# Optimization experiments

Hardware: AMD Instinct MI355X
Metric: run time of the kernel (lower is better)

The kernel has to match this reference:

```python
import math
import jax, jax.numpy as jnp
import numpy as np
from jax import lax

MUL = 16           # multiplicity of 0e and 1o in input and output irreps
NRB = 8            # num_radial_basis
DIAMETER = 3.0
STEPS = (1.0, 1.0, 1.0)
DIM = 4 * MUL      # 16 scalars + 16 vectors * 3 = 64 channels


def _constants():
    # lattice from __init__: arange(-s, s+1) * step per axis, s = floor(r/step)
    r = DIAMETER / 2
    axes = [np.arange(-math.floor(r / st), math.floor(r / st) + 1.0) * st for st in STEPS]
    lattice = np.stack(np.meshgrid(*axes, indexing='ij'), axis=-1)  # [Kx,Ky,Kz,3]
    d = np.linalg.norm(lattice, axis=-1)                            # [Kx,Ky,Kz]
    # soft_one_hot_linspace(basis='smooth_finite', cutoff=True)
    values = np.linspace(0.0, r, NRB + 2)[1:-1]
    step = values[1] - values[0]
    diff = (d[..., None] - values) / step
    inside = diff ** 2 < 1.0
    emb = np.where(inside, 1.14136 * np.exp(2.0) * np.exp(-2.0 / np.where(inside, 1.0 - diff ** 2, 1.0)), 0.0)
    # spherical harmonics, normalize=True, normalization='component'
    n = lattice / np.maximum(d[..., None], 1e-12)  # unit vectors; 0 at the origin voxel
    sh0 = np.ones_like(d)                          # Y_0 (component normalized)
    sh1 = np.sqrt(3.0) * n                         # Y_1 (component normalized)
    return emb.astype(np.float32), sh0.astype(np.float32), sh1.astype(np.float32)

EMB, SH0, SH1 = _constants()
KX, KY, KZ = SH0.shape  # 3,3,3


def setup_inputs() -> dict:
    key = jax.random.key(0)
    ks = jax.random.split(key, 7)
    B, G = 4, 32
    return {
        'x': jax.random.normal(ks[0], (B, G, G, G, DIM), jnp.float32),
        'W_sc0': jax.random.normal(ks[1], (MUL, MUL), jnp.float32),  # Linear 0e->0e
        'W_sc1': jax.random.normal(ks[2], (MUL, MUL), jnp.float32),  # Linear 1o->1o
        'w1': jax.random.normal(ks[3], (NRB, MUL, MUL), jnp.float32),  # path 0e x 0e -> 0e
        'w2': jax.random.normal(ks[4], (NRB, MUL, MUL), jnp.float32),  # path 0e x 1o -> 1o
        'w3': jax.random.normal(ks[5], (NRB, MUL, MUL), jnp.float32),  # path 1o x 0e -> 1o
        'w4': jax.random.normal(ks[6], (NRB, MUL, MUL), jnp.float32),  # path 1o x 1o -> 0e
    }


def _kernel(w1, w2, w3, w4):
    # radial basis -> per-voxel path weights, divided by kernel volume (as in source)
    emb, sh0, sh1 = jnp.asarray(EMB), jnp.asarray(SH0), jnp.asarray(SH1)
    norm = float(KX * KY * KZ)
    W1, W2, W3, W4 = [jnp.einsum('xyzk,kio->xyzio', emb, w) / norm for w in (w1, w2, w3, w4)]
    # path normalization: each output irrep receives 2 paths of fan_in mul*1 = 16 -> 1/sqrt(32)
    alpha = 1.0 / np.sqrt(2.0 * MUL)
    # tp.right blocks (Clebsch-Gordan contractions, lmax=1):
    k00 = alpha * W1 * sh0[..., None, None]                                              # [.,i,o]
    k01 = alpha * jnp.einsum('xyzio,xyzm->xyziom', W2, sh1).reshape(KX, KY, KZ, MUL, 3 * MUL)
    k10 = (alpha / np.sqrt(3.0)) * jnp.einsum('xyzio,xyzm->xyzimo', W4, sh1).reshape(KX, KY, KZ, 3 * MUL, MUL)
    k11 = alpha * jnp.einsum('xyzio,mn->xyzimon', W3 * sh0[..., None, None],
                             jnp.eye(3, dtype=W3.dtype)).reshape(KX, KY, KZ, 3 * MUL, 3 * MUL)
    return jnp.concatenate([jnp.concatenate([k00, k01], axis=-1),
                            jnp.concatenate([k10, k11], axis=-1)], axis=-2)  # [Kx,Ky,Kz,64,64]


def reference(x, W_sc0, W_sc1, w1, w2, w3, w4):
    B, X, Y, Z, _ = x.shape
    inv_sqrt_mul = 1.0 / np.sqrt(MUL)
    # self-connection: e3nn Linear per irrep (applied pointwise over b,x,y,z)
    xs = x[..., :MUL]                                   # [B,X,Y,Z,16] scalars
    xv = x[..., MUL:].reshape(B, X, Y, Z, MUL, 3)       # [B,X,Y,Z,16,3] vectors
    sc_s = (xs @ W_sc0) * inv_sqrt_mul
    sc_v = jnp.einsum('bxyzic,io->bxyzoc', xv, W_sc1) * inv_sqrt_mul
    sc = jnp.concatenate([sc_s, sc_v.reshape(B, X, Y, Z, 3 * MUL)], axis=-1)
    # position-dependent equivariant kernel + standard 3D conv
    k = _kernel(w1, w2, w3, w4)
    conv = lax.conv_general_dilated(x, k, (1, 1, 1), 'SAME',
                                    dimension_numbers=('NXYZC', 'XYZIO', 'NXYZC'))
    return sc + conv
```

## Files before the change

### kernel.cpp

```cpp
#include <hip/hip_runtime.h>

typedef unsigned short u16;
typedef unsigned int u32;
typedef __bf16 bf16x8 __attribute__((ext_vector_type(8)));
typedef float f32x4 __attribute__((ext_vector_type(4)));
typedef u32 u32x4 __attribute__((ext_vector_type(4)));

__device__ __align__(16) u16 g_kTr[27 * 8 * 512];

__device__ __forceinline__ u32 pack_bf(float a, float b) {
    u32 ua = __float_as_uint(a) + 0x8000u;
    u32 ub = __float_as_uint(b) + 0x8000u;
    return __builtin_amdgcn_perm(ub, ua, 0x07060302u);
}

__global__ __launch_bounds__(64) void build_k(
    const float* __restrict__ Wsc0, const float* __restrict__ Wsc1,
    const float* __restrict__ w1, const float* __restrict__ w2,
    const float* __restrict__ w3, const float* __restrict__ w4)
{
    const int t = blockIdx.x;
    const int c = threadIdx.x;
    const int dx = t / 9 - 1, dy = (t / 3) % 3 - 1, dz = t % 3 - 1;
    const float d = sqrtf((float)(dx * dx + dy * dy + dz * dz));
    const float step = 1.5f / 9.0f;
    float emb[8];
#pragma unroll
    for (int k = 0; k < 8; ++k) {
        float diff = (d - (float)(k + 1) * step) / step;
        float q = diff * diff;
        emb[k] = (q < 1.0f) ? 1.14136f * expf(2.0f - 2.0f / (1.0f - q)) : 0.0f;
    }
    const float dn = fmaxf(d, 1e-12f);
    const float s3 = 1.7320508075688772f;
    const float sh1[3] = { s3 * dx / dn, s3 * dy / dn, s3 * dz / dn };
    const float alpha  = 0.17677669529663687f;
    const float alpha3 = alpha * 0.57735026918962576f;

    const int base2 = ((t * 2 + (c >> 5)) * 2 + ((c >> 4) & 1)) * 2;
    const int l15c  = c & 15;
    auto put = [&](int r, float v) {
        u32 u = __float_as_uint(v);
        u += 0x7FFFu + ((u >> 16) & 1u);
        g_kTr[(base2 + (r >> 5)) * 512 + (((r >> 3) & 3) * 16 + l15c) * 8 + (r & 7)] =
            (u16)(u >> 16);
    };

    if (c < 16) {
        const int o = c;
#pragma unroll
        for (int i = 0; i < 16; ++i) {
            float W1 = 0.f, W4 = 0.f;
#pragma unroll
            for (int k = 0; k < 8; ++k) {
                W1 += emb[k] * w1[k * 256 + i * 16 + o];
                W4 += emb[k] * w4[k * 256 + i * 16 + o];
            }
            W1 *= (1.0f / 27.0f); W4 *= (1.0f / 27.0f);
            float v0 = alpha * W1;
            if (t == 13) v0 += 0.25f * Wsc0[i * 16 + o];
            put(i, v0);
            const float base = alpha3 * W4;
#pragma unroll
            for (int m = 0; m < 3; ++m) put(16 + 3 * i + m, base * sh1[m]);
        }
    } else {
        const int o = (c - 16) / 3, nc = (c - 16) % 3;
#pragma unroll
        for (int i = 0; i < 16; ++i) {
            float W2 = 0.f, W3 = 0.f;
#pragma unroll
            for (int k = 0; k < 8; ++k) {
                W2 += emb[k] * w2[k * 256 + i * 16 + o];
                W3 += emb[k] * w3[k * 256 + i * 16 + o];
            }
            W2 *= (1.0f / 27.0f); W3 *= (1.0f / 27.0f);
            put(i, alpha * W2 * sh1[nc]);
#pragma unroll
            for (int m = 0; m < 3; ++m) {
                float v = (m == nc) ? alpha * W3 : 0.0f;
                if (t == 13 && m == nc) v += 0.25f * Wsc1[i * 16 + o];
                put(16 + 3 * i + m, v);
            }
        }
    }
}

#define BUFU16 39424

#define WALL() __builtin_amdgcn_sched_barrier(0);

#define LOADB(S, T) { \
  const u32x4* _p = reinterpret_cast<const u32x4*>(bTr + (T) * 8192); \
  B##S##0 = _p[0]; B##S##1 = _p[64]; B##S##2 = _p[128]; B##S##3 = _p[192]; }

#define LOADA2(s, i0, i1, RCC) { \
  const int _r  = rbase + (RCC); \
  const int _o0 = _r * 128 + ((kg ^ (_r & 7)) << 4); \
  A##s##_##i0 = *reinterpret_cast<const bf16x8*>(abase + _o0); \
  A##s##_##i1 = *reinterpret_cast<const bf16x8*>(abase + (_o0 ^ 64)); }

#define RCC4(T, YY, MT) ((((T)/9)*6 + (YY) + (((T)/3)%3))*34 + ((T)%3) + (MT)*16)

#define LOAD_A8(s, T) \
  LOADA2(s, 0, 1, RCC4(T,0,0)) \
  LOADA2(s, 2, 3, RCC4(T,0,1)) \
  LOADA2(s, 4, 5, RCC4(T,1,0)) \
  LOADA2(s, 6, 7, RCC4(T,1,1))

#define SLD(S, C) { \
  const int _c   = wv * 20 + (C); \
  const int _row = _c * 8 + rloc; \
  const int _rid = _row / 204; \
  const int _rem = _row - _rid * 204; \
  const int _yi  = _rem / 34; \
  const int _zid = _rem - _yi * 34; \
  const int _xin = Xs + _rid - 1; \
  const int _yin = ys0 + _yi - 1; \
  const int _zin = _zid - 1; \
  const bool _ib = (_row < 612) && ((unsigned)_xin < 32u) && \
                   ((unsigned)_yin < 32u) && ((unsigned)_zin < 32u); \
  F##S##a = (f32x4){0.f, 0.f, 0.f, 0.f}; \
  F##S##b = (f32x4){0.f, 0.f, 0.f, 0.f}; \
  if (_ib) { \
    const f32x4* _p = reinterpret_cast<const f32x4*>( \
        x + ((size_t)(((bs * 32 + _xin) * 32 + _yin) * 32 + _zin) * 64 + swz * 8)); \
    F##S##a = _p[0]; F##S##b = _p[1]; \
  } }

#define SWR(S, C) { \
  const int _c = wv * 20 + (C); \
  if (_c < 77) { \
    u32x4 _pk; \
    _pk[0] = pack_bf(F##S##a[0], F##S##a[1]); \
    _pk[1] = pack_bf(F##S##a[2], F##S##a[3]); \
    _pk[2] = pack_bf(F##S##b[0], F##S##b[1]); \
    _pk[3] = pack_bf(F##S##b[2], F##S##b[3]); \
    *reinterpret_cast<u32x4*>(bufn + _c * 512 + lane * 8) = _pk; \
  } }

#define BC(x) __builtin_bit_cast(bf16x8, x)
#define MF(b_, a_, c_) __builtin_amdgcn_mfma_f32_16x16x32_bf16(BC(b_), a_, c_, 0, 0, 0)

#define MFMA16(bs, as) \
  acc000 = MF(B##bs##0, A##as##_0, acc000); acc001 = MF(B##bs##2, A##as##_0, acc001); \
  acc010 = MF(B##bs##0, A##as##_2, acc010); acc011 = MF(B##bs##2, A##as##_2, acc011); \
  acc100 = MF(B##bs##0, A##as##_4, acc100); acc101 = MF(B##bs##2, A##as##_4, acc101); \
  acc110 = MF(B##bs##0, A##as##_6, acc110); acc111 = MF(B##bs##2, A##as##_6, acc111); \
  acc000 = MF(B##bs##1, A##as##_1, acc000); acc001 = MF(B##bs##3, A##as##_1, acc001); \
  acc010 = MF(B##bs##1, A##as##_3, acc010); acc011 = MF(B##bs##3, A##as##_3, acc011); \
  acc100 = MF(B##bs##1, A##as##_5, acc100); acc101 = MF(B##bs##3, A##as##_5, acc101); \
  acc110 = MF(B##bs##1, A##as##_7, acc110); acc111 = MF(B##bs##3, A##as##_7, acc111);

__global__ __launch_bounds__(256, 1) void conv_mfma11(
    const float* __restrict__ x, float* __restrict__ out)
{
    extern __shared__ u16 xt[];

    const int blk   = blockIdx.x;
    const int tbase = ((blk & 7) * 32 + (blk >> 3)) * 4;
    const int tid   = threadIdx.x;
    const int wv    = tid >> 6;
    const int lane  = tid & 63;
    const int l15   = lane & 15;
    const int kg    = lane >> 4;
    const int yh    = wv >> 1;
    const int nh    = wv & 1;
    const int rloc  = lane >> 3;
    const int swz   = (lane & 7) ^ rloc;
    const int rbase = yh * 68 + l15;

    const char* bTr = (const char*)g_kTr + nh * 4096 + lane * 16;

    u32x4 B00, B01, B02, B03, B10, B11, B12, B13, B20, B21, B22, B23;
    bf16x8 A0_0, A0_1, A0_2, A0_3, A0_4, A0_5, A0_6, A0_7;
    bf16x8 A1_0, A1_1, A1_2, A1_3, A1_4, A1_5, A1_6, A1_7;
    f32x4 F0a, F0b, F1a, F1b, F2a, F2b, F3a, F3b;

    {
        const int ts = tbase;
        const int bs = ts >> 8, Xs = (ts >> 3) & 31, ys0 = (ts & 7) << 2;
        u16* bufn = xt;
#pragma unroll
        for (int g = 0; g < 5; ++g) {
            SLD(0, g * 4 + 0) SLD(1, g * 4 + 1) SLD(2, g * 4 + 2) SLD(3, g * 4 + 3)
            SWR(0, g * 4 + 0) SWR(1, g * 4 + 1) SWR(2, g * 4 + 2) SWR(3, g * 4 + 3)
        }
    }
    __syncthreads();

#pragma unroll 1
    for (int k = 0; k < 4; ++k) {
        const u16* bufk = xt + (k & 1) * BUFU16;
        u16*       bufn = xt + ((k & 1) ^ 1) * BUFU16;
        const char* abase = (const char*)bufk;

        const int tk = tbase + k;
        const int b  = tk >> 8, X = (tk >> 3) & 31, y0 = (tk & 7) << 2;
        const int ts = tbase + (k < 3 ? k + 1 : 3);
        const int bs = ts >> 8, Xs = (ts >> 3) & 31, ys0 = (ts & 7) << 2;

        const f32x4 z4 = {0.f, 0.f, 0.f, 0.f};
        f32x4 acc000 = z4, acc001 = z4, acc010 = z4, acc011 = z4;
        f32x4 acc100 = z4, acc101 = z4, acc110 = z4, acc111 = z4;

        LOADB(0, 1) LOADB(1, 3) LOAD_A8(0, 1)
        WALL()
        SLD(0,0)  SLD(1,1)              LOADB(2, 4)  LOAD_A8(1, 3)  MFMA16(0, 0) WALL()
        SLD(2,2)  SLD(3,3)              LOADB(0, 5)  LOAD_A8(0, 4)  MFMA16(1, 1) WALL()
        SWR(0,0)  SWR(1,1)  SLD(0,4)  SLD(1,5)   LOADB(1, 7)  LOAD_A8(1, 5)  MFMA16(2, 0) WALL()
        SWR(2,2)  SWR(3,3)  SLD(2,6)  SLD(3,7)   LOADB(2, 9)  LOAD_A8(0, 7)  MFMA16(0, 1) WALL()
        SWR(0,4)  SWR(1,5)  SLD(0,8)  SLD(1,9)   LOADB(0, 10) LOAD_A8(1, 9)  MFMA16(1, 0) WALL()
        SWR(2,6)  SWR(3,7)  SLD(2,10) SLD(3,11)  LOADB(1, 11) LOAD_A8(0, 10) MFMA16(2, 1) WALL()
        SWR(0,8)  SWR(1,9)  SLD(0,12) SLD(1,13)  LOADB(2, 12) LOAD_A8(1, 11) MFMA16(0, 0) WALL()
        SWR(2,10) SWR(3,11) SLD(2,14) SLD(3,15)  LOADB(0, 13) LOAD_A8(0, 12) MFMA16(1, 1) WALL()
        SWR(0,12) SWR(1,13) SLD(0,16) SLD(1,17)  LOADB(1, 14) LOAD_A8(1, 13) MFMA16(2, 0) WALL()
        SWR(2,14) SWR(3,15) SLD(2,18) SLD(3,19)  LOADB(2, 15) LOAD_A8(0, 14) MFMA16(0, 1) WALL()
        SWR(0,16) SWR(1,17)                      LOADB(0, 16) LOAD_A8(1, 15) MFMA16(1, 0) WALL()
        SWR(2,18) SWR(3,19)                      LOADB(1, 17) LOAD_A8(0, 16) MFMA16(2, 1) WALL()
                                                 LOADB(2, 19) LOAD_A8(1, 17) MFMA16(0, 0) WALL()
                                                 LOADB(0, 21) LOAD_A8(0, 19) MFMA16(1, 1) WALL()
                                                 LOADB(1, 22) LOAD_A8(1, 21) MFMA16(2, 0) WALL()
                                                 LOADB(2, 23) LOAD_A8(0, 22) MFMA16(0, 1) WALL()
                                                 LOADB(0, 25) LOAD_A8(1, 23) MFMA16(1, 0) WALL()
                                                              LOAD_A8(0, 25) MFMA16(2, 1) WALL()
                                                                             MFMA16(0, 0) WALL()

        float* obase = out + (((size_t)(b * 32 + X) * 32 + (y0 + yh * 2)) * 32) * 64
                     + nh * 32 + kg * 4;
        *reinterpret_cast<f32x4*>(obase + l15 * 64)                    = acc000;
        *reinterpret_cast<f32x4*>(obase + l15 * 64 + 16)               = acc001;
        *reinterpret_cast<f32x4*>(obase + (16 + l15) * 64)             = acc010;
        *reinterpret_cast<f32x4*>(obase + (16 + l15) * 64 + 16)        = acc011;
        *reinterpret_cast<f32x4*>(obase + 2048 + l15 * 64)             = acc100;
        *reinterpret_cast<f32x4*>(obase + 2048 + l15 * 64 + 16)        = acc101;
        *reinterpret_cast<f32x4*>(obase + 2048 + (16 + l15) * 64)      = acc110;
        *reinterpret_cast<f32x4*>(obase + 2048 + (16 + l15) * 64 + 16) = acc111;

        __syncthreads();
    }
}

extern "C" void kernel_launch(void* const* d_in, const int* in_sizes, int n_in,
                              void* d_out, int out_size, void* d_ws, size_t ws_size,
                              hipStream_t stream)
{
    const float* x    = (const float*)d_in[0];
    const float* Wsc0 = (const float*)d_in[1];
    const float* Wsc1 = (const float*)d_in[2];
    const float* w1   = (const float*)d_in[3];
    const float* w2   = (const float*)d_in[4];
    const float* w3   = (const float*)d_in[5];
    const float* w4   = (const float*)d_in[6];
    float* out = (float*)d_out;

    build_k<<<dim3(27), dim3(64), 0, stream>>>(Wsc0, Wsc1, w1, w2, w3, w4);
    conv_mfma11<<<dim3(256), dim3(256), 2 * 78848, stream>>>(x, out);
}
```

Baseline: 54.59 us.

## Double wavefronts per block, halving per-wave output rows and staging work

Launches the conv kernel with 512 threads (8 waves) instead of 256. Each wave now computes one y-row of outputs instead of two, with half the accumulators and A-fragment registers, and stages half as many input chunks into LDS. The aim is more waves per CU to hide LDS and global latency, and lower per-wave register pressure. The cost is that each B fragment is loaded by twice as many waves, so redundant kernel-weight loads double and MFMA work per wave is thinner.

```diff
diff --git a/kernel.cpp b/kernel.cpp
--- a/kernel.cpp
+++ b/kernel.cpp
@@ -100,16 +100,14 @@
   A##s##_##i0 = *reinterpret_cast<const bf16x8*>(abase + _o0); \
   A##s##_##i1 = *reinterpret_cast<const bf16x8*>(abase + (_o0 ^ 64)); }
 
-#define RCC4(T, YY, MT) ((((T)/9)*6 + (YY) + (((T)/3)%3))*34 + ((T)%3) + (MT)*16)
-
-#define LOAD_A8(s, T) \
-  LOADA2(s, 0, 1, RCC4(T,0,0)) \
-  LOADA2(s, 2, 3, RCC4(T,0,1)) \
-  LOADA2(s, 4, 5, RCC4(T,1,0)) \
-  LOADA2(s, 6, 7, RCC4(T,1,1))
+#define RCCW(T, MT) ((((T)/9)*6 + (((T)/3)%3))*34 + ((T)%3) + (MT)*16)
+
+#define LOAD_A4(s, T) \
+  LOADA2(s, 0, 1, RCCW(T,0)) \
+  LOADA2(s, 2, 3, RCCW(T,1))
 
 #define SLD(S, C) { \
-  const int _c   = wv * 20 + (C); \
+  const int _c   = wv * 10 + (C); \
   const int _row = _c * 8 + rloc; \
   const int _rid = _row / 204; \
   const int _rem = _row - _rid * 204; \
@@ -129,7 +127,7 @@
   } }
 
 #define SWR(S, C) { \
-  const int _c = wv * 20 + (C); \
+  const int _c = wv * 10 + (C); \
   if (_c < 77) { \
     u32x4 _pk; \
     _pk[0] = pack_bf(F##S##a[0], F##S##a[1]); \
@@ -142,17 +140,13 @@
 #define BC(x) __builtin_bit_cast(bf16x8, x)
 #define MF(b_, a_, c_) __builtin_amdgcn_mfma_f32_16x16x32_bf16(BC(b_), a_, c_, 0, 0, 0)
 
-#define MFMA16(bs, as) \
-  acc000 = MF(B##bs##0, A##as##_0, acc000); acc001 = MF(B##bs##2, A##as##_0, acc001); \
-  acc010 = MF(B##bs##0, A##as##_2, acc010); acc011 = MF(B##bs##2, A##as##_2, acc011); \
-  acc100 = MF(B##bs##0, A##as##_4, acc100); acc101 = MF(B##bs##2, A##as##_4, acc101); \
-  acc110 = MF(B##bs##0, A##as##_6, acc110); acc111 = MF(B##bs##2, A##as##_6, acc111); \
-  acc000 = MF(B##bs##1, A##as##_1, acc000); acc001 = MF(B##bs##3, A##as##_1, acc001); \
-  acc010 = MF(B##bs##1, A##as##_3, acc010); acc011 = MF(B##bs##3, A##as##_3, acc011); \
-  acc100 = MF(B##bs##1, A##as##_5, acc100); acc101 = MF(B##bs##3, A##as##_5, acc101); \
-  acc110 = MF(B##bs##1, A##as##_7, acc110); acc111 = MF(B##bs##3, A##as##_7, acc111);
-
-__global__ __launch_bounds__(256, 1) void conv_mfma11(
+#define MFMA8(bs, as) \
+  acc00 = MF(B##bs##0, A##as##_0, acc00); acc01 = MF(B##bs##2, A##as##_0, acc01); \
+  acc10 = MF(B##bs##0, A##as##_2, acc10); acc11 = MF(B##bs##2, A##as##_2, acc11); \
+  acc00 = MF(B##bs##1, A##as##_1, acc00); acc01 = MF(B##bs##3, A##as##_1, acc01); \
+  acc10 = MF(B##bs##1, A##as##_3, acc10); acc11 = MF(B##bs##3, A##as##_3, acc11);
+
+__global__ __launch_bounds__(512, 1) void conv_mfma12(
     const float* __restrict__ x, float* __restrict__ out)
 {
     extern __shared__ u16 xt[];
@@ -168,14 +162,14 @@
     const int nh    = wv & 1;
     const int rloc  = lane >> 3;
     const int swz   = (lane & 7) ^ rloc;
-    const int rbase = yh * 68 + l15;
+    const int rbase = yh * 34 + l15;
 
     const char* bTr = (const char*)g_kTr + nh * 4096 + lane * 16;
 
     u32x4 B00, B01, B02, B03, B10, B11, B12, B13, B20, B21, B22, B23;
-    bf16x8 A0_0, A0_1, A0_2, A0_3, A0_4, A0_5, A0_6, A0_7;
-    bf16x8 A1_0, A1_1, A1_2, A1_3, A1_4, A1_5, A1_6, A1_7;
-    f32x4 F0a, F0b, F1a, F1b, F2a, F2b, F3a, F3b;
+    bf16x8 A0_0, A0_1, A0_2, A0_3;
+    bf16x8 A1_0, A1_1, A1_2, A1_3;
+    f32x4 F0a, F0b, F1a, F1b, F2a, F2b;
 
     {
         const int ts = tbase;
@@ -183,8 +177,8 @@
         u16* bufn = xt;
 #pragma unroll
         for (int g = 0; g < 5; ++g) {
-            SLD(0, g * 4 + 0) SLD(1, g * 4 + 1) SLD(2, g * 4 + 2) SLD(3, g * 4 + 3)
-            SWR(0, g * 4 + 0) SWR(1, g * 4 + 1) SWR(2, g * 4 + 2) SWR(3, g * 4 + 3)
+            SLD(0, g * 2 + 0) SLD(1, g * 2 + 1)
+            SWR(0, g * 2 + 0) SWR(1, g * 2 + 1)
         }
     }
     __syncthreads();
@@ -201,41 +195,36 @@
         const int bs = ts >> 8, Xs = (ts >> 3) & 31, ys0 = (ts & 7) << 2;
 
         const f32x4 z4 = {0.f, 0.f, 0.f, 0.f};
-        f32x4 acc000 = z4, acc001 = z4, acc010 = z4, acc011 = z4;
-        f32x4 acc100 = z4, acc101 = z4, acc110 = z4, acc111 = z4;
-
-        LOADB(0, 1) LOADB(1, 3) LOAD_A8(0, 1)
+        f32x4 acc00 = z4, acc01 = z4, acc10 = z4, acc11 = z4;
+
+        LOADB(0, 1) LOADB(1, 3) LOAD_A4(0, 1)
         WALL()
-        SLD(0,0)  SLD(1,1)              LOADB(2, 4)  LOAD_A8(1, 3)  MFMA16(0, 0) WALL()
-        SLD(2,2)  SLD(3,3)              LOADB(0, 5)  LOAD_A8(0, 4)  MFMA16(1, 1) WALL()
-        SWR(0,0)  SWR(1,1)  SLD(0,4)  SLD(1,5)   LOADB(1, 7)  LOAD_A8(1, 5)  MFMA16(2, 0) WALL()
-        SWR(2,2)  SWR(3,3)  SLD(2,6)  SLD(3,7)   LOADB(2, 9)  LOAD_A8(0, 7)  MFMA16(0, 1) WALL()
-        SWR(0,4)  SWR(1,5)  SLD(0,8)  SLD(1,9)   LOADB(0, 10) LOAD_A8(1, 9)  MFMA16(1, 0) WALL()
-        SWR(2,6)  SWR(3,7)  SLD(2,10) SLD(3,11)  LOADB(1, 11) LOAD_A8(0, 10) MFMA16(2, 1) WALL()
-        SWR(0,8)  SWR(1,9)  SLD(0,12) SLD(1,13)  LOADB(2, 12) LOAD_A8(1, 11) MFMA16(0, 0) WALL()
-        SWR(2,10) SWR(3,11) SLD(2,14) SLD(3,15)  LOADB(0, 13) LOAD_A8(0, 12) MFMA16(1, 1) WALL()
-        SWR(0,12) SWR(1,13) SLD(0,16) SLD(1,17)  LOADB(1, 14) LOAD_A8(1, 13) MFMA16(2, 0) WALL()
-        SWR(2,14) SWR(3,15) SLD(2,18) SLD(3,19)  LOADB(2, 15) LOAD_A8(0, 14) MFMA16(0, 1) WALL()
-        SWR(0,16) SWR(1,17)                      LOADB(0, 16) LOAD_A8(1, 15) MFMA16(1, 0) WALL()
-        SWR(2,18) SWR(3,19)                      LOADB(1, 17) LOAD_A8(0, 16) MFMA16(2, 1) WALL()
-                                                 LOADB(2, 19) LOAD_A8(1, 17) MFMA16(0, 0) WALL()
-                                                 LOADB(0, 21) LOAD_A8(0, 19) MFMA16(1, 1) WALL()
-                                                 LOADB(1, 22) LOAD_A8(1, 21) MFMA16(2, 0) WALL()
-                                                 LOADB(2, 23) LOAD_A8(0, 22) MFMA16(0, 1) WALL()
-                                                 LOADB(0, 25) LOAD_A8(1, 23) MFMA16(1, 0) WALL()
-                                                              LOAD_A8(0, 25) MFMA16(2, 1) WALL()
-                                                                             MFMA16(0, 0) WALL()
-
-        float* obase = out + (((size_t)(b * 32 + X) * 32 + (y0 + yh * 2)) * 32) * 64
+        SLD(0,0)           LOADB(2, 4)  LOAD_A4(1, 3)  MFMA8(0, 0) WALL()
+        SLD(1,1)           LOADB(0, 5)  LOAD_A4(0, 4)  MFMA8(1, 1) WALL()
+        SLD(2,2) SWR(0,0)  LOADB(1, 7)  LOAD_A4(1, 5)  MFMA8(2, 0) WALL()
+        SLD(0,3) SWR(1,1)  LOADB(2, 9)  LOAD_A4(0, 7)  MFMA8(0, 1) WALL()
+        SLD(1,4) SWR(2,2)  LOADB(0, 10) LOAD_A4(1, 9)  MFMA8(1, 0) WALL()
+        SLD(2,5) SWR(0,3)  LOADB(1, 11) LOAD_A4(0, 10) MFMA8(2, 1) WALL()
+        SLD(0,6) SWR(1,4)  LOADB(2, 12) LOAD_A4(1, 11) MFMA8(0, 0) WALL()
+        SLD(1,7) SWR(2,5)  LOADB(0, 13) LOAD_A4(0, 12) MFMA8(1, 1) WALL()
+        SLD(2,8) SWR(0,6)  LOADB(1, 14) LOAD_A4(1, 13) MFMA8(2, 0) WALL()
+        SLD(0,9) SWR(1,7)  LOADB(2, 15) LOAD_A4(0, 14) MFMA8(0, 1) WALL()
+                 SWR(2,8)  LOADB(0, 16) LOAD_A4(1, 15) MFMA8(1, 0) WALL()
+                 SWR(0,9)  LOADB(1, 17) LOAD_A4(0, 16) MFMA8(2, 1) WALL()
+                           LOADB(2, 19) LOAD_A4(1, 17) MFMA8(0, 0) WALL()
+                           LOADB(0, 21) LOAD_A4(0, 19) MFMA8(1, 1) WALL()
+                           LOADB(1, 22) LOAD_A4(1, 21) MFMA8(2, 0) WALL()
+                           LOADB(2, 23) LOAD_A4(0, 22) MFMA8(0, 1) WALL()
+                           LOADB(0, 25) LOAD_A4(1, 23) MFMA8(1, 0) WALL()
+                                        LOAD_A4(0, 25) MFMA8(2, 1) WALL()
+                                                       MFMA8(0, 0) WALL()
+
+        float* obase = out + (((size_t)(b * 32 + X) * 32 + (y0 + yh)) * 32) * 64
                      + nh * 32 + kg * 4;
-        *reinterpret_cast<f32x4*>(obase + l15 * 64)                    = acc000;
-        *reinterpret_cast<f32x4*>(obase + l15 * 64 + 16)               = acc001;
-        *reinterpret_cast<f32x4*>(obase + (16 + l15) * 64)             = acc010;
-        *reinterpret_cast<f32x4*>(obase + (16 + l15) * 64 + 16)        = acc011;
-        *reinterpret_cast<f32x4*>(obase + 2048 + l15 * 64)             = acc100;
-        *reinterpret_cast<f32x4*>(obase + 2048 + l15 * 64 + 16)        = acc101;
-        *reinterpret_cast<f32x4*>(obase + 2048 + (16 + l15) * 64)      = acc110;
-        *reinterpret_cast<f32x4*>(obase + 2048 + (16 + l15) * 64 + 16) = acc111;
+        *reinterpret_cast<f32x4*>(obase + l15 * 64)             = acc00;
+        *reinterpret_cast<f32x4*>(obase + l15 * 64 + 16)        = acc01;
+        *reinterpret_cast<f32x4*>(obase + (16 + l15) * 64)      = acc10;
+        *reinterpret_cast<f32x4*>(obase + (16 + l15) * 64 + 16) = acc11;
 
         __syncthreads();
     }
@@ -255,5 +244,5 @@
     float* out = (float*)d_out;
 
     build_k<<<dim3(27), dim3(64), 0, stream>>>(Wsc0, Wsc1, w1, w2, w3, w4);
-    conv_mfma11<<<dim3(256), dim3(256), 2 * 78848, stream>>>(x, out);
-}
+    conv_mfma12<<<dim3(256), dim3(512), 2 * 78848, stream>>>(x, out);
+}
```

Result: slower. 138.4 us (+153.4%).
